# Kernel tuning notes

Measured on AMD Instinct MI355X. Metric: run time of the kernel, lower is better.

Reference implementation:

```python
import jax, jax.numpy as jnp
import numpy as np

N = 100000      # nodes
E = 1600000     # edges
IN = 64         # in_channels
ED = 16         # edge_dim
HID = 64        # hidden_dim
L = 5           # num conv layers
MLPL = 4        # linears per GINE mlp
B = 512         # num graphs
BN_EPS = 1e-5


def _linear_init(key, fan_in, shape):
    bound = 1.0 / np.sqrt(fan_in)
    return jax.random.uniform(key, shape, jnp.float32, -bound, bound)


def setup_inputs() -> dict:
    key = jax.random.key(0)
    ks = jax.random.split(key, 12)
    x = jax.random.normal(ks[0], (N, IN), jnp.float32)
    edge_index = jax.random.randint(ks[1], (2, E), 0, N)
    batch = jnp.sort(jax.random.randint(ks[2], (N,), 0, B))
    edge_attr = jax.random.normal(ks[3], (E, ED), jnp.float32)

    node_W = _linear_init(ks[4], IN, (IN, HID))
    node_b = _linear_init(ks[5], IN, (HID,))
    edge_W = _linear_init(ks[6], ED, (ED, HID))
    edge_b = _linear_init(ks[7], ED, (HID,))
    eps_arr = jnp.zeros((L,), jnp.float32)           # train_eps init = 0
    mlp_W = _linear_init(ks[8], HID, (L, MLPL, HID, HID))
    mlp_b = _linear_init(ks[9], HID, (L, MLPL, HID))
    bn_gamma = jnp.ones((L, HID), jnp.float32)
    bn_beta = jnp.zeros((L, HID), jnp.float32)

    return dict(x=x, edge_attr=edge_attr, node_W=node_W, node_b=node_b,
                edge_W=edge_W, edge_b=edge_b, eps_arr=eps_arr,
                mlp_W=mlp_W, mlp_b=mlp_b, bn_gamma=bn_gamma, bn_beta=bn_beta,
                edge_index=edge_index, batch=batch)


def _mlp(h, Ws, bs):
    # Linear,ReLU,Linear,ReLU,Linear,ReLU,Linear (make_mlp num_layers=4)
    for i in range(MLPL):
        h = h @ Ws[i] + bs[i]
        if i < MLPL - 1:
            h = jax.nn.relu(h)
    return h


def reference(x, edge_attr, node_W, node_b, edge_W, edge_b, eps_arr,
              mlp_W, mlp_b, bn_gamma, bn_beta, edge_index, batch):
    h = x @ node_W + node_b                      # [N, HID]
    e = edge_attr @ edge_W + edge_b              # [E, HID]
    src, dst = edge_index[0], edge_index[1]      # messages src -> dst
    for l in range(L):
        h_res = h
        msg = jax.nn.relu(h[src] + e)            # [E, HID] GINE message
        aggr = jax.ops.segment_sum(msg, dst, num_segments=N)
        h = _mlp((1.0 + eps_arr[l]) * h + aggr, mlp_W[l], mlp_b[l])
        mu = h.mean(axis=0)
        var = h.var(axis=0)                      # biased, matches BN training
        h = (h - mu) * jax.lax.rsqrt(var + BN_EPS) * bn_gamma[l] + bn_beta[l]
        h = jax.nn.relu(h) + h_res
    # global mean pool
    counts = jax.ops.segment_sum(jnp.ones((h.shape[0],), h.dtype), batch, num_segments=B)
    g = jax.ops.segment_sum(h, batch, num_segments=B) / jnp.clip(counts, 1.0)[:, None]
    return g
```

## Files before the change

### kernel.cpp

```cpp
#include <hip/hip_runtime.h>

typedef unsigned short u16;
typedef unsigned int u32;
typedef __attribute__((ext_vector_type(8))) short short8_t;
typedef __attribute__((ext_vector_type(4))) float f32x4;

static_assert(sizeof(short8_t) == 16, "short8 must be 16B");

#define NN 100000
#define NE 1600000

__device__ __forceinline__ float b2f(u16 s) {
    return __builtin_bit_cast(float, ((u32)s) << 16);
}
__device__ __forceinline__ u16 f2b(float f) {
    u32 u = __builtin_bit_cast(u32, f);
    u32 r = u + 0x7fffu + ((u >> 16) & 1u);
    return (u16)(r >> 16);
}
__device__ __forceinline__ u32 pack2(float a, float b) {
    return (u32)f2b(a) | ((u32)f2b(b) << 16);
}
__device__ __forceinline__ float ldf(const void* p, size_t i, int bf) {
    return bf ? b2f(((const u16*)p)[i]) : ((const float*)p)[i];
}

__global__ void detect_kernel(const u32* __restrict__ g, int* __restrict__ flag) {
    if (threadIdx.x == 0 && blockIdx.x == 0) flag[0] = (g[0] == 0x3F803F80u) ? 1 : 0;
}

__global__ __launch_bounds__(256) void hist_kernel(const int* __restrict__ dstA,
                                                   int* __restrict__ cnt, int ne) {
    int e = blockIdx.x * 256 + threadIdx.x;
    if (e >= ne) return;
    atomicAdd(&cnt[dstA[e]], 1);
}

__global__ __launch_bounds__(256) void scanA_kernel(const int* __restrict__ cnt,
                                                    int* __restrict__ tmp,
                                                    int* __restrict__ bsum, int n) {
    __shared__ int sm[2][512];
    int t = threadIdx.x;
    int b0 = blockIdx.x * 512;
    sm[0][t] = (b0 + t < n) ? cnt[b0 + t] : 0;
    sm[0][t + 256] = (b0 + t + 256 < n) ? cnt[b0 + t + 256] : 0;
    int pp = 0;
    for (int off = 1; off < 512; off <<= 1) {
        __syncthreads();
        int j0 = t, j1 = t + 256;
        sm[pp ^ 1][j0] = sm[pp][j0] + (j0 >= off ? sm[pp][j0 - off] : 0);
        sm[pp ^ 1][j1] = sm[pp][j1] + (j1 >= off ? sm[pp][j1 - off] : 0);
        pp ^= 1;
    }
    __syncthreads();
    if (b0 + t < n) tmp[b0 + t] = sm[pp][t];
    if (b0 + t + 256 < n) tmp[b0 + t + 256] = sm[pp][t + 256];
    if (t == 0) bsum[blockIdx.x] = sm[pp][511];
}

__global__ __launch_bounds__(256) void scanB_kernel(int* __restrict__ bsum, int nb) {
    __shared__ int sm[2][256];
    int t = threadIdx.x;
    sm[0][t] = (t < nb) ? bsum[t] : 0;
    int pp = 0;
    for (int off = 1; off < 256; off <<= 1) {
        __syncthreads();
        sm[pp ^ 1][t] = sm[pp][t] + (t >= off ? sm[pp][t - off] : 0);
        pp ^= 1;
    }
    __syncthreads();
    bsum[t] = (t == 0) ? 0 : sm[pp][t - 1];
}

__global__ __launch_bounds__(256) void scanC_kernel(const int* __restrict__ tmp,
                                                    const int* __restrict__ bsum,
                                                    int* __restrict__ row_start, int n, int ne) {
    int i = blockIdx.x * 256 + threadIdx.x;
    if (i > n) return;
    if (i == n) { row_start[n] = ne; return; }
    int off = bsum[i >> 9];
    int loc = i & 511;
    row_start[i] = off + (loc ? tmp[i - 1] : 0);
}

__global__ __launch_bounds__(256) void scatter_kernel(const int* __restrict__ srcA,
                                                      const int* __restrict__ dstA,
                                                      int* __restrict__ cursor,
                                                      int* __restrict__ sperm,
                                                      int* __restrict__ eidx, int ne) {
    int e = blockIdx.x * 256 + threadIdx.x;
    if (e >= ne) return;
    int d = dstA[e];
    int pos = atomicAdd(&cursor[d], 1);
    sperm[pos] = srcA[e];
    eidx[pos] = e;
}

__global__ __launch_bounds__(256) void eperm_kernel(const void* __restrict__ edge_attr,
                                                    const void* __restrict__ eW,
                                                    const void* __restrict__ eB,
                                                    const int* __restrict__ eidx,
                                                    u16* __restrict__ ec, int ne,
                                                    const int* __restrict__ flagp) {
    int bf = flagp[0];
    int lane = threadIdx.x & 63;
    int m = lane & 15;
    int quad = lane >> 4;
    int wid = (blockIdx.x * 256 + threadIdx.x) >> 6;
    int nw = gridDim.x * 4;
    short8_t bfr[4];
    float bsv[4];
#pragma unroll
    for (int t = 0; t < 4; t++) {
        short8_t f;
#pragma unroll
        for (int j = 0; j < 8; j++) {
            int k = quad * 8 + j;
            u16 wv = 0;
            if (k < 16) wv = f2b(ldf(eW, (size_t)k * 64 + t * 16 + m, bf));
            f[j] = (short)wv;
        }
        bfr[t] = f;
        bsv[t] = ldf(eB, t * 16 + m, bf);
    }
    int ngroups = (ne + 15) >> 4;
    for (int g = wid; g < ngroups; g += nw) {
        int row = g * 16 + m;
        int eid = (row < ne) ? eidx[row] : 0;
        short8_t afr = {0, 0, 0, 0, 0, 0, 0, 0};
        if (quad < 2) {
            if (bf) {
                const u16* ap = (const u16*)edge_attr + (size_t)eid * 16 + quad * 8;
                afr = *(const short8_t*)ap;
            } else {
                const float* ap = (const float*)edge_attr + (size_t)eid * 16 + quad * 8;
                float4 q0 = *(const float4*)ap;
                float4 q1 = *(const float4*)(ap + 4);
                afr[0] = (short)f2b(q0.x); afr[1] = (short)f2b(q0.y);
                afr[2] = (short)f2b(q0.z); afr[3] = (short)f2b(q0.w);
                afr[4] = (short)f2b(q1.x); afr[5] = (short)f2b(q1.y);
                afr[6] = (short)f2b(q1.z); afr[7] = (short)f2b(q1.w);
            }
        }
        f32x4 acc[4];
#pragma unroll
        for (int t = 0; t < 4; t++) {
            f32x4 a;
            a[0] = bsv[t]; a[1] = bsv[t]; a[2] = bsv[t]; a[3] = bsv[t];
            acc[t] = __builtin_amdgcn_mfma_f32_16x16x32_bf16(afr, bfr[t], a, 0, 0, 0);
        }
        int rbase = g * 16 + quad * 4;
#pragma unroll
        for (int t = 0; t < 4; t++)
#pragma unroll
            for (int r = 0; r < 4; r++) {
                int rr = rbase + r;
                if (rr < ne) ec[(size_t)rr * 64 + t * 16 + m] = f2b(acc[t][r]);
            }
    }
}

__global__ __launch_bounds__(256) void eacopy_kernel(const void* __restrict__ edge_attr,
                                                     const int* __restrict__ eidx,
                                                     u16* __restrict__ eap, int ne,
                                                     const int* __restrict__ flagp) {
    int bf = flagp[0];
    long long t = (long long)blockIdx.x * 256 + threadIdx.x;
    if (t >= (long long)ne * 16) return;
    int j = (int)(t >> 4), c = (int)(t & 15);
    int eid = eidx[j];
    eap[(size_t)j * 16 + c] = f2b(ldf(edge_attr, (size_t)eid * 16 + c, bf));
}

template <int NLIN, bool STATS, bool INEXT, bool OUTB16>
__global__ __launch_bounds__(256) void linear64_kernel(const void* in, float* out, u16* outb,
                                                       const void* __restrict__ W, size_t w_off,
                                                       const void* __restrict__ bias,
                                                       size_t b_off, float* stats, int n,
                                                       const int* __restrict__ flagp) {
    __shared__ __align__(16) u16 Ab[2][64 * 72];
    const int bf = flagp[0];
    const int tid = threadIdx.x;
    const int lane = tid & 63;
    const int w = tid >> 6;
    const int m = lane & 15;
    const int quad = lane >> 4;
    const int col = w * 16 + m;
    short8_t bfr[NLIN][2];
    float bsv[NLIN];
#pragma unroll
    for (int i = 0; i < NLIN; i++) {
        bsv[i] = ldf(bias, b_off + i * 64 + col, bf);
#pragma unroll
        for (int kk = 0; kk < 2; kk++) {
            short8_t f;
#pragma unroll
            for (int j = 0; j < 8; j++) {
                size_t idx = w_off + (size_t)i * 4096 + (size_t)(kk * 32 + quad * 8 + j) * 64 + col;
                u16 wv = bf ? ((const u16*)W)[idx] : f2b(((const float*)W)[idx]);
                f[j] = (short)wv;
            }
            bfr[i][kk] = f;
        }
    }
    const int srow = tid >> 2;
    const int sc0 = (tid & 3) << 4;
    const int ntiles = (n + 63) >> 6;
    for (int tile = blockIdx.x; tile < ntiles; tile += gridDim.x) {
        const int base = tile * 64;
        __syncthreads();
        {
            int gr = base + srow;
            uint4 w0 = make_uint4(0, 0, 0, 0), w1 = make_uint4(0, 0, 0, 0);
            if (gr < n) {
                if (INEXT && bf) {
                    const uint4* gp = (const uint4*)((const u16*)in + (size_t)gr * 64 + sc0);
                    w0 = gp[0];
                    w1 = gp[1];
                } else {
                    const float4* gp = (const float4*)((const float*)in + (size_t)gr * 64 + sc0);
                    float4 q0 = gp[0], q1 = gp[1], q2 = gp[2], q3 = gp[3];
                    w0.x = pack2(q0.x, q0.y); w0.y = pack2(q0.z, q0.w);
                    w0.z = pack2(q1.x, q1.y); w0.w = pack2(q1.z, q1.w);
                    w1.x = pack2(q2.x, q2.y); w1.y = pack2(q2.z, q2.w);
                    w1.z = pack2(q3.x, q3.y); w1.w = pack2(q3.z, q3.w);
                }
            }
            uint4* lp = (uint4*)&Ab[0][srow * 72 + sc0];
            lp[0] = w0;
            lp[1] = w1;
        }
        __syncthreads();
        int cur = 0;
#pragma unroll
        for (int i = 0; i < NLIN; i++) {
            f32x4 accT[4];
#pragma unroll
            for (int t = 0; t < 4; t++) {
                f32x4 acc;
                acc[0] = bsv[i]; acc[1] = bsv[i]; acc[2] = bsv[i]; acc[3] = bsv[i];
                int r = t * 16 + m;
                const u16* ap = &Ab[cur][r * 72 + quad * 8];
                short8_t a0 = *(const short8_t*)ap;
                short8_t a1 = *(const short8_t*)(ap + 32);
                acc = __builtin_amdgcn_mfma_f32_16x16x32_bf16(a0, bfr[i][0], acc, 0, 0, 0);
                acc = __builtin_amdgcn_mfma_f32_16x16x32_bf16(a1, bfr[i][1], acc, 0, 0, 0);
                accT[t] = acc;
            }
            if (i < NLIN - 1) {
#pragma unroll
                for (int t = 0; t < 4; t++)
#pragma unroll
                    for (int reg = 0; reg < 4; reg++) {
                        int r2 = t * 16 + quad * 4 + reg;
                        Ab[cur ^ 1][r2 * 72 + col] = f2b(fmaxf(accT[t][reg], 0.f));
                    }
                __syncthreads();
                cur ^= 1;
            } else {
                float s1 = 0.f, s2 = 0.f;
#pragma unroll
                for (int t = 0; t < 4; t++)
#pragma unroll
                    for (int reg = 0; reg < 4; reg++) {
                        int gr = base + t * 16 + quad * 4 + reg;
                        if (gr < n) {
                            float v = accT[t][reg];
                            out[(size_t)gr * 64 + col] = v;
                            if (OUTB16) outb[(size_t)gr * 64 + col] = f2b(v);
                            if (STATS) { s1 += v; s2 += v * v; }
                        }
                    }
                if (STATS) {
                    s1 += __shfl_xor(s1, 16, 64);
                    s2 += __shfl_xor(s2, 16, 64);
                    s1 += __shfl_xor(s1, 32, 64);
                    s2 += __shfl_xor(s2, 32, 64);
                    if (quad == 0) {
                        atomicAdd(&stats[col], s1);
                        atomicAdd(&stats[64 + col], s2);
                    }
                }
            }
        }
    }
}

template <bool EC>
__global__ __launch_bounds__(256) void agg_kernel(const float* __restrict__ h,
                                                  const u16* __restrict__ hb,
                                                  const u16* __restrict__ ec,
                                                  const int* __restrict__ sperm,
                                                  const int* __restrict__ row_start,
                                                  const void* __restrict__ eps_arr, int layer,
                                                  float* __restrict__ u, int n,
                                                  const void* __restrict__ eW,
                                                  const void* __restrict__ eB,
                                                  const int* __restrict__ flagp) {
    int bf = flagp[0];
    int lane = threadIdx.x & 63;
    int i = blockIdx.x * 4 + (threadIdx.x >> 6);
    if (i >= n) return;
    float wt[16];
    float ebv = 0.f;
    if (!EC) {
#pragma unroll
        for (int k = 0; k < 16; k++) wt[k] = ldf(eW, k * 64 + lane, bf);
        ebv = ldf(eB, lane, bf);
    }
    int beg = row_start[i], end = row_start[i + 1];
    float acc = 0.f;
    if (EC) {
        int p = beg;
        for (; p + 3 < end; p += 4) {
            int s0 = sperm[p], s1 = sperm[p + 1], s2 = sperm[p + 2], s3 = sperm[p + 3];
            float h0 = b2f(hb[(size_t)s0 * 64 + lane]);
            float h1 = b2f(hb[(size_t)s1 * 64 + lane]);
            float h2 = b2f(hb[(size_t)s2 * 64 + lane]);
            float h3 = b2f(hb[(size_t)s3 * 64 + lane]);
            float e0 = b2f(ec[(size_t)p * 64 + lane]);
            float e1 = b2f(ec[(size_t)(p + 1) * 64 + lane]);
            float e2 = b2f(ec[(size_t)(p + 2) * 64 + lane]);
            float e3 = b2f(ec[(size_t)(p + 3) * 64 + lane]);
            acc += fmaxf(h0 + e0, 0.f);
            acc += fmaxf(h1 + e1, 0.f);
            acc += fmaxf(h2 + e2, 0.f);
            acc += fmaxf(h3 + e3, 0.f);
        }
        for (; p < end; ++p) {
            int s0 = sperm[p];
            acc += fmaxf(b2f(hb[(size_t)s0 * 64 + lane]) + b2f(ec[(size_t)p * 64 + lane]), 0.f);
        }
    } else {
        for (int p = beg; p < end; ++p) {
            int s0 = sperm[p];
            float hv = b2f(hb[(size_t)s0 * 64 + lane]);
            float eav = 0.f;
            if (lane < 16) eav = b2f(ec[(size_t)p * 16 + lane]);
            float ev = ebv;
#pragma unroll
            for (int k = 0; k < 16; k++) {
                int bits = __builtin_amdgcn_readlane(__builtin_bit_cast(int, eav), k);
                ev += __builtin_bit_cast(float, bits) * wt[k];
            }
            acc += fmaxf(hv + ev, 0.f);
        }
    }
    float eps = 1.f + ldf(eps_arr, layer, bf);
    u[(size_t)i * 64 + lane] = eps * h[(size_t)i * 64 + lane] + acc;
}

__global__ __launch_bounds__(256) void bnres_kernel(const float* __restrict__ v,
                                                    float* __restrict__ h, u16* __restrict__ hb,
                                                    const float* __restrict__ stats,
                                                    const void* __restrict__ gamma,
                                                    const void* __restrict__ beta, size_t g_off,
                                                    int n, const int* __restrict__ flagp) {
    int bf = flagp[0];
    size_t base = ((size_t)blockIdx.x * 256 + threadIdx.x) * 4;
    if (base >= (size_t)n * 64) return;
    int f0 = (int)(base & 63);
    float inv = 1.f / (float)n;
    float4 vv = *(const float4*)(v + base);
    float4 hh = *(const float4*)(h + base);
    float vs[4] = {vv.x, vv.y, vv.z, vv.w};
    float hs[4] = {hh.x, hh.y, hh.z, hh.w};
    float res[4];
    u16 pb[4];
#pragma unroll
    for (int j = 0; j < 4; j++) {
        int f = f0 + j;
        float mu = stats[f] * inv;
        float var = stats[64 + f] * inv - mu * mu;
        float rs = rsqrtf(var + 1e-5f);
        float ga = ldf(gamma, g_off + f, bf), be = ldf(beta, g_off + f, bf);
        float y = (vs[j] - mu) * rs * ga + be;
        float hn = fmaxf(y, 0.f) + hs[j];
        res[j] = hn;
        pb[j] = f2b(hn);
    }
    float4 ro;
    ro.x = res[0]; ro.y = res[1]; ro.z = res[2]; ro.w = res[3];
    *(float4*)(h + base) = ro;
    uint2 po;
    po.x = (u32)pb[0] | ((u32)pb[1] << 16);
    po.y = (u32)pb[2] | ((u32)pb[3] << 16);
    *(uint2*)(hb + base) = po;
}

__global__ __launch_bounds__(256) void pool1_kernel(const float* __restrict__ h,
                                                    const int* __restrict__ batch,
                                                    float* __restrict__ gsum,
                                                    float* __restrict__ gcnt, int n) {
    int lane = threadIdx.x & 63;
    int s = blockIdx.x * 4 + (threadIdx.x >> 6);
    int start = s * 256;
    if (start >= n) return;
    int endn = min(start + 256, n);
    int cur = -1;
    float acc = 0.f, c = 0.f;
    for (int m = start; m < endn; ++m) {
        int b = batch[m];
        if (b != cur) {
            if (cur >= 0) {
                atomicAdd(&gsum[cur * 64 + lane], acc);
                if (lane == 0) atomicAdd(&gcnt[cur], c);
            }
            cur = b;
            acc = 0.f;
            c = 0.f;
        }
        acc += h[(size_t)m * 64 + lane];
        c += 1.f;
    }
    if (cur >= 0) {
        atomicAdd(&gsum[cur * 64 + lane], acc);
        if (lane == 0) atomicAdd(&gcnt[cur], c);
    }
}

__global__ __launch_bounds__(256) void pool2_kernel(const float* __restrict__ gsum,
                                                    const float* __restrict__ gcnt,
                                                    float* __restrict__ out) {
    int idx = blockIdx.x * 256 + threadIdx.x;
    if (idx >= 512 * 64) return;
    int b = idx >> 6;
    out[idx] = gsum[idx] / fmaxf(gcnt[b], 1.f);
}

extern "C" void kernel_launch(void* const* d_in, const int* in_sizes, int n_in, void* d_out,
                              int out_size, void* d_ws, size_t ws_size, hipStream_t stream) {
    const int N = NN, E = NE;
    const void* x = d_in[0];
    const void* edge_attr = d_in[1];
    const void* node_W = d_in[2];
    const void* node_b = d_in[3];
    const void* edge_W = d_in[4];
    const void* edge_b = d_in[5];
    const void* eps_arr = d_in[6];
    const void* mlp_W = d_in[7];
    const void* mlp_b = d_in[8];
    const void* bn_gamma = d_in[9];
    const void* bn_beta = d_in[10];
    const int* edge_index = (const int*)d_in[11];
    const int* batch = (const int*)d_in[12];

    char* ws = (char*)d_ws;
    size_t o = 0;
    auto take = [&](size_t bytes) -> size_t {
        size_t r = o;
        o = (o + bytes + 255) & ~(size_t)255;
        return r;
    };
    size_t cnt_o = take((size_t)N * 4);
    size_t stats_o = take(5 * 128 * 4);
    size_t gsum_o = take(512 * 64 * 4);
    size_t gcnt_o = take(512 * 4);
    size_t zero_len = o;
    size_t flag_o = take(256);
    size_t row_o = take((size_t)(N + 1) * 4);
    size_t tmp_o = take((size_t)N * 4);
    size_t bsum_o = take(256 * 4);
    size_t cur_o = take((size_t)N * 4);
    size_t sperm_o = take((size_t)E * 4);
    size_t eidx_o = take((size_t)E * 4);
    size_t h_o = take((size_t)N * 64 * 4);
    size_t hb_o = take((size_t)N * 64 * 2);
    size_t u_o = take((size_t)N * 64 * 4);
    size_t ec_o = o;
    bool EC = ws_size >= ec_o + (size_t)E * 64 * 2;

    int* cnt = (int*)(ws + cnt_o);
    float* stats = (float*)(ws + stats_o);
    float* gsum = (float*)(ws + gsum_o);
    float* gcnt = (float*)(ws + gcnt_o);
    int* flagp = (int*)(ws + flag_o);
    int* row = (int*)(ws + row_o);
    int* tmp = (int*)(ws + tmp_o);
    int* bsum = (int*)(ws + bsum_o);
    int* curs = (int*)(ws + cur_o);
    int* sperm = (int*)(ws + sperm_o);
    int* eidx = (int*)(ws + eidx_o);
    float* h = (float*)(ws + h_o);
    u16* hb = (u16*)(ws + hb_o);
    float* u = (float*)(ws + u_o);
    u16* ecache = (u16*)(ws + ec_o);

    hipMemsetAsync(ws, 0, zero_len, stream);
    detect_kernel<<<1, 64, 0, stream>>>((const u32*)bn_gamma, flagp);
    const int* srcA = edge_index;
    const int* dstA = edge_index + E;

    hist_kernel<<<E / 256, 256, 0, stream>>>(dstA, cnt, E);
    int nb = (N + 511) / 512;
    scanA_kernel<<<nb, 256, 0, stream>>>(cnt, tmp, bsum, N);
    scanB_kernel<<<1, 256, 0, stream>>>(bsum, nb);
    scanC_kernel<<<(N + 256) / 256, 256, 0, stream>>>(tmp, bsum, row, N, E);
    hipMemcpyAsync(curs, row, (size_t)N * 4, hipMemcpyDeviceToDevice, stream);
    scatter_kernel<<<E / 256, 256, 0, stream>>>(srcA, dstA, curs, sperm, eidx, E);

    if (EC)
        eperm_kernel<<<2048, 256, 0, stream>>>(edge_attr, edge_W, edge_b, eidx, ecache, E, flagp);
    else
        eacopy_kernel<<<(E * 16) / 256, 256, 0, stream>>>(edge_attr, eidx, ecache, E, flagp);

    linear64_kernel<1, false, true, true><<<784, 256, 0, stream>>>(
        x, h, hb, node_W, 0, node_b, 0, nullptr, N, flagp);

    for (int l = 0; l < 5; l++) {
        if (EC)
            agg_kernel<true><<<N / 4, 256, 0, stream>>>(h, hb, ecache, sperm, row, eps_arr, l, u,
                                                        N, edge_W, edge_b, flagp);
        else
            agg_kernel<false><<<N / 4, 256, 0, stream>>>(h, hb, ecache, sperm, row, eps_arr, l, u,
                                                         N, edge_W, edge_b, flagp);
        linear64_kernel<4, true, false, false><<<784, 256, 0, stream>>>(
            u, u, nullptr, mlp_W, (size_t)l * 4 * 4096, mlp_b, (size_t)l * 256,
            stats + l * 128, N, flagp);
        bnres_kernel<<<(N * 64 / 4 + 255) / 256, 256, 0, stream>>>(
            u, h, hb, stats + l * 128, bn_gamma, bn_beta, (size_t)l * 64, N, flagp);
    }

    pool1_kernel<<<(N + 1023) / 1024, 256, 0, stream>>>(h, batch, gsum, gcnt, N);
    pool2_kernel<<<(512 * 64) / 256, 256, 0, stream>>>(gsum, gcnt, (float*)d_out);
}
```

Measured before the change: 1.629 ms.

## Switch aggregation to edge-balanced chunks with atomic boundary merges

The per-node aggregation kernel becomes an edge-parallel kernel. Each wave handles a fixed chunk of dst-sorted edges, accumulates runs with the same destination, and merges chunk-boundary partial sums with atomics. The (1+eps)*h self term is now written ahead of time into u by the producing kernel (node linear or BN-residual), which lets aggregation accumulate in place. Smaller changes fold the cursor copy into the scan kernel and process two edge groups per iteration in the edge-projection kernel. The aim is load balance independent of node degree; the cost is an extra dperm array, atomic traffic, and extra writes of u.

```diff
diff --git a/kernel.cpp b/kernel.cpp
--- a/kernel.cpp
+++ b/kernel.cpp
@@ -9,6 +9,7 @@
 
 #define NN 100000
 #define NE 1600000
+#define CH 128
 
 __device__ __forceinline__ float b2f(u16 s) {
     return __builtin_bit_cast(float, ((u32)s) << 16);
@@ -74,26 +75,64 @@
 
 __global__ __launch_bounds__(256) void scanC_kernel(const int* __restrict__ tmp,
                                                     const int* __restrict__ bsum,
-                                                    int* __restrict__ row_start, int n, int ne) {
+                                                    int* __restrict__ row_start,
+                                                    int* __restrict__ curs, int n, int ne) {
     int i = blockIdx.x * 256 + threadIdx.x;
     if (i > n) return;
     if (i == n) { row_start[n] = ne; return; }
     int off = bsum[i >> 9];
     int loc = i & 511;
-    row_start[i] = off + (loc ? tmp[i - 1] : 0);
+    int v = off + (loc ? tmp[i - 1] : 0);
+    row_start[i] = v;
+    curs[i] = v;
 }
 
 __global__ __launch_bounds__(256) void scatter_kernel(const int* __restrict__ srcA,
                                                       const int* __restrict__ dstA,
                                                       int* __restrict__ cursor,
                                                       int* __restrict__ sperm,
+                                                      int* __restrict__ dperm,
                                                       int* __restrict__ eidx, int ne) {
     int e = blockIdx.x * 256 + threadIdx.x;
     if (e >= ne) return;
     int d = dstA[e];
     int pos = atomicAdd(&cursor[d], 1);
     sperm[pos] = srcA[e];
+    dperm[pos] = d;
     eidx[pos] = e;
+}
+
+__device__ __forceinline__ short8_t load_afr(const void* __restrict__ edge_attr,
+                                             const int* __restrict__ eidx, int row, int ne,
+                                             int quad, int bf) {
+    short8_t afr = {0, 0, 0, 0, 0, 0, 0, 0};
+    int eid = (row < ne) ? eidx[row] : 0;
+    if (quad < 2) {
+        if (bf) {
+            afr = *(const short8_t*)((const u16*)edge_attr + (size_t)eid * 16 + quad * 8);
+        } else {
+            const float* ap = (const float*)edge_attr + (size_t)eid * 16 + quad * 8;
+            float4 q0 = *(const float4*)ap;
+            float4 q1 = *(const float4*)(ap + 4);
+            afr[0] = (short)f2b(q0.x); afr[1] = (short)f2b(q0.y);
+            afr[2] = (short)f2b(q0.z); afr[3] = (short)f2b(q0.w);
+            afr[4] = (short)f2b(q1.x); afr[5] = (short)f2b(q1.y);
+            afr[6] = (short)f2b(q1.z); afr[7] = (short)f2b(q1.w);
+        }
+    }
+    return afr;
+}
+
+__device__ __forceinline__ void store_ec(u16* __restrict__ ec, const f32x4* acc, int g, int quad,
+                                         int m, int ne) {
+    int rbase = g * 16 + quad * 4;
+#pragma unroll
+    for (int t = 0; t < 4; t++)
+#pragma unroll
+        for (int r = 0; r < 4; r++) {
+            int rr = rbase + r;
+            if (rr < ne) ec[(size_t)rr * 64 + t * 16 + m] = f2b(acc[t][r]);
+        }
 }
 
 __global__ __launch_bounds__(256) void eperm_kernel(const void* __restrict__ edge_attr,
@@ -124,39 +163,23 @@
         bsv[t] = ldf(eB, t * 16 + m, bf);
     }
     int ngroups = (ne + 15) >> 4;
-    for (int g = wid; g < ngroups; g += nw) {
-        int row = g * 16 + m;
-        int eid = (row < ne) ? eidx[row] : 0;
-        short8_t afr = {0, 0, 0, 0, 0, 0, 0, 0};
-        if (quad < 2) {
-            if (bf) {
-                const u16* ap = (const u16*)edge_attr + (size_t)eid * 16 + quad * 8;
-                afr = *(const short8_t*)ap;
-            } else {
-                const float* ap = (const float*)edge_attr + (size_t)eid * 16 + quad * 8;
-                float4 q0 = *(const float4*)ap;
-                float4 q1 = *(const float4*)(ap + 4);
-                afr[0] = (short)f2b(q0.x); afr[1] = (short)f2b(q0.y);
-                afr[2] = (short)f2b(q0.z); afr[3] = (short)f2b(q0.w);
-                afr[4] = (short)f2b(q1.x); afr[5] = (short)f2b(q1.y);
-                afr[6] = (short)f2b(q1.z); afr[7] = (short)f2b(q1.w);
-            }
-        }
-        f32x4 acc[4];
+    int npairs = (ngroups + 1) >> 1;
+    for (int gp = wid; gp < npairs; gp += nw) {
+        int ga = gp * 2, gb = gp * 2 + 1;
+        short8_t afrA = load_afr(edge_attr, eidx, ga * 16 + m, ne, quad, bf);
+        short8_t afrB = {0, 0, 0, 0, 0, 0, 0, 0};
+        bool hasB = (gb < ngroups);
+        if (hasB) afrB = load_afr(edge_attr, eidx, gb * 16 + m, ne, quad, bf);
+        f32x4 accA[4], accB[4];
 #pragma unroll
         for (int t = 0; t < 4; t++) {
             f32x4 a;
             a[0] = bsv[t]; a[1] = bsv[t]; a[2] = bsv[t]; a[3] = bsv[t];
-            acc[t] = __builtin_amdgcn_mfma_f32_16x16x32_bf16(afr, bfr[t], a, 0, 0, 0);
-        }
-        int rbase = g * 16 + quad * 4;
-#pragma unroll
-        for (int t = 0; t < 4; t++)
-#pragma unroll
-            for (int r = 0; r < 4; r++) {
-                int rr = rbase + r;
-                if (rr < ne) ec[(size_t)rr * 64 + t * 16 + m] = f2b(acc[t][r]);
-            }
+            accA[t] = __builtin_amdgcn_mfma_f32_16x16x32_bf16(afrA, bfr[t], a, 0, 0, 0);
+            accB[t] = __builtin_amdgcn_mfma_f32_16x16x32_bf16(afrB, bfr[t], a, 0, 0, 0);
+        }
+        store_ec(ec, accA, ga, quad, m, ne);
+        if (hasB) store_ec(ec, accB, gb, quad, m, ne);
     }
 }
 
@@ -172,12 +195,15 @@
     eap[(size_t)j * 16 + c] = f2b(ldf(edge_attr, (size_t)eid * 16 + c, bf));
 }
 
-template <int NLIN, bool STATS, bool INEXT, bool OUTB16>
+template <int NLIN, bool STATS, bool INEXT, bool OUTB16, bool UINIT>
 __global__ __launch_bounds__(256) void linear64_kernel(const void* in, float* out, u16* outb,
                                                        const void* __restrict__ W, size_t w_off,
                                                        const void* __restrict__ bias,
                                                        size_t b_off, float* stats, int n,
-                                                       const int* __restrict__ flagp) {
+                                                       const int* __restrict__ flagp,
+                                                       float* uinit,
+                                                       const void* __restrict__ eps_arr,
+                                                       int eps_idx) {
     __shared__ __align__(16) u16 Ab[2][64 * 72];
     const int bf = flagp[0];
     const int tid = threadIdx.x;
@@ -186,6 +212,8 @@
     const int m = lane & 15;
     const int quad = lane >> 4;
     const int col = w * 16 + m;
+    float epsv = 0.f;
+    if (UINIT) epsv = 1.f + ldf(eps_arr, eps_idx, bf);
     short8_t bfr[NLIN][2];
     float bsv[NLIN];
 #pragma unroll
@@ -268,6 +296,7 @@
                             float v = accT[t][reg];
                             out[(size_t)gr * 64 + col] = v;
                             if (OUTB16) outb[(size_t)gr * 64 + col] = f2b(v);
+                            if (UINIT) uinit[(size_t)gr * 64 + col] = epsv * v;
                             if (STATS) { s1 += v; s2 += v * v; }
                         }
                     }
@@ -286,86 +315,114 @@
     }
 }
 
-template <bool EC>
-__global__ __launch_bounds__(256) void agg_kernel(const float* __restrict__ h,
-                                                  const u16* __restrict__ hb,
-                                                  const u16* __restrict__ ec,
-                                                  const int* __restrict__ sperm,
-                                                  const int* __restrict__ row_start,
-                                                  const void* __restrict__ eps_arr, int layer,
-                                                  float* __restrict__ u, int n,
-                                                  const void* __restrict__ eW,
-                                                  const void* __restrict__ eB,
-                                                  const int* __restrict__ flagp) {
+__global__ __launch_bounds__(256) void agg2_kernel(const u16* __restrict__ hb,
+                                                   const u16* __restrict__ ec,
+                                                   const int* __restrict__ sperm,
+                                                   const int* __restrict__ dperm,
+                                                   float* u, int ne) {
+    int lane = threadIdx.x & 63;
+    int wv = blockIdx.x * 4 + (threadIdx.x >> 6);
+    int p0 = wv * CH;
+    if (p0 >= ne) return;
+    int pend = min(p0 + CH, ne);
+    int cur = dperm[p0];
+    float acc = 0.f;
+    bool first = true;
+    int p = p0;
+    for (; p + 3 < pend; p += 4) {
+        int4 s4 = *(const int4*)(sperm + p);
+        int4 d4 = *(const int4*)(dperm + p);
+        float hv[4], ev[4];
+        hv[0] = b2f(hb[(size_t)s4.x * 64 + lane]);
+        hv[1] = b2f(hb[(size_t)s4.y * 64 + lane]);
+        hv[2] = b2f(hb[(size_t)s4.z * 64 + lane]);
+        hv[3] = b2f(hb[(size_t)s4.w * 64 + lane]);
+        ev[0] = b2f(ec[(size_t)p * 64 + lane]);
+        ev[1] = b2f(ec[(size_t)(p + 1) * 64 + lane]);
+        ev[2] = b2f(ec[(size_t)(p + 2) * 64 + lane]);
+        ev[3] = b2f(ec[(size_t)(p + 3) * 64 + lane]);
+        int ds[4] = {d4.x, d4.y, d4.z, d4.w};
+#pragma unroll
+        for (int j = 0; j < 4; j++) {
+            if (ds[j] != cur) {
+                float* up = &u[(size_t)cur * 64 + lane];
+                if (first) atomicAdd(up, acc);
+                else *up += acc;
+                first = false;
+                cur = ds[j];
+                acc = 0.f;
+            }
+            acc += fmaxf(hv[j] + ev[j], 0.f);
+        }
+    }
+    for (; p < pend; ++p) {
+        int s = sperm[p], d = dperm[p];
+        if (d != cur) {
+            float* up = &u[(size_t)cur * 64 + lane];
+            if (first) atomicAdd(up, acc);
+            else *up += acc;
+            first = false;
+            cur = d;
+            acc = 0.f;
+        }
+        acc += fmaxf(b2f(hb[(size_t)s * 64 + lane]) + b2f(ec[(size_t)p * 64 + lane]), 0.f);
+    }
+    atomicAdd(&u[(size_t)cur * 64 + lane], acc);
+}
+
+__global__ __launch_bounds__(256) void aggF_kernel(const u16* __restrict__ hb,
+                                                   const u16* __restrict__ ec,
+                                                   const int* __restrict__ sperm,
+                                                   const int* __restrict__ row_start,
+                                                   float* u, int n,
+                                                   const void* __restrict__ eW,
+                                                   const void* __restrict__ eB,
+                                                   const int* __restrict__ flagp) {
     int bf = flagp[0];
     int lane = threadIdx.x & 63;
     int i = blockIdx.x * 4 + (threadIdx.x >> 6);
     if (i >= n) return;
     float wt[16];
-    float ebv = 0.f;
-    if (!EC) {
-#pragma unroll
-        for (int k = 0; k < 16; k++) wt[k] = ldf(eW, k * 64 + lane, bf);
-        ebv = ldf(eB, lane, bf);
-    }
+#pragma unroll
+    for (int k = 0; k < 16; k++) wt[k] = ldf(eW, k * 64 + lane, bf);
+    float ebv = ldf(eB, lane, bf);
     int beg = row_start[i], end = row_start[i + 1];
     float acc = 0.f;
-    if (EC) {
-        int p = beg;
-        for (; p + 3 < end; p += 4) {
-            int s0 = sperm[p], s1 = sperm[p + 1], s2 = sperm[p + 2], s3 = sperm[p + 3];
-            float h0 = b2f(hb[(size_t)s0 * 64 + lane]);
-            float h1 = b2f(hb[(size_t)s1 * 64 + lane]);
-            float h2 = b2f(hb[(size_t)s2 * 64 + lane]);
-            float h3 = b2f(hb[(size_t)s3 * 64 + lane]);
-            float e0 = b2f(ec[(size_t)p * 64 + lane]);
-            float e1 = b2f(ec[(size_t)(p + 1) * 64 + lane]);
-            float e2 = b2f(ec[(size_t)(p + 2) * 64 + lane]);
-            float e3 = b2f(ec[(size_t)(p + 3) * 64 + lane]);
-            acc += fmaxf(h0 + e0, 0.f);
-            acc += fmaxf(h1 + e1, 0.f);
-            acc += fmaxf(h2 + e2, 0.f);
-            acc += fmaxf(h3 + e3, 0.f);
-        }
-        for (; p < end; ++p) {
-            int s0 = sperm[p];
-            acc += fmaxf(b2f(hb[(size_t)s0 * 64 + lane]) + b2f(ec[(size_t)p * 64 + lane]), 0.f);
-        }
-    } else {
-        for (int p = beg; p < end; ++p) {
-            int s0 = sperm[p];
-            float hv = b2f(hb[(size_t)s0 * 64 + lane]);
-            float eav = 0.f;
-            if (lane < 16) eav = b2f(ec[(size_t)p * 16 + lane]);
-            float ev = ebv;
-#pragma unroll
-            for (int k = 0; k < 16; k++) {
-                int bits = __builtin_amdgcn_readlane(__builtin_bit_cast(int, eav), k);
-                ev += __builtin_bit_cast(float, bits) * wt[k];
-            }
-            acc += fmaxf(hv + ev, 0.f);
-        }
-    }
-    float eps = 1.f + ldf(eps_arr, layer, bf);
-    u[(size_t)i * 64 + lane] = eps * h[(size_t)i * 64 + lane] + acc;
-}
-
-__global__ __launch_bounds__(256) void bnres_kernel(const float* __restrict__ v,
-                                                    float* __restrict__ h, u16* __restrict__ hb,
+    for (int p = beg; p < end; ++p) {
+        int s0 = sperm[p];
+        float hv = b2f(hb[(size_t)s0 * 64 + lane]);
+        float eav = 0.f;
+        if (lane < 16) eav = b2f(ec[(size_t)p * 16 + lane]);
+        float ev = ebv;
+#pragma unroll
+        for (int k = 0; k < 16; k++) {
+            int bits = __builtin_amdgcn_readlane(__builtin_bit_cast(int, eav), k);
+            ev += __builtin_bit_cast(float, bits) * wt[k];
+        }
+        acc += fmaxf(hv + ev, 0.f);
+    }
+    u[(size_t)i * 64 + lane] += acc;
+}
+
+__global__ __launch_bounds__(256) void bnres_kernel(float* uv, float* __restrict__ h,
+                                                    u16* __restrict__ hb,
                                                     const float* __restrict__ stats,
                                                     const void* __restrict__ gamma,
                                                     const void* __restrict__ beta, size_t g_off,
-                                                    int n, const int* __restrict__ flagp) {
+                                                    int n, const int* __restrict__ flagp,
+                                                    const void* __restrict__ eps_arr,
+                                                    int eps_next, int write_u) {
     int bf = flagp[0];
     size_t base = ((size_t)blockIdx.x * 256 + threadIdx.x) * 4;
     if (base >= (size_t)n * 64) return;
     int f0 = (int)(base & 63);
     float inv = 1.f / (float)n;
-    float4 vv = *(const float4*)(v + base);
+    float epsv = write_u ? (1.f + ldf(eps_arr, eps_next, bf)) : 0.f;
+    float4 vv = *(const float4*)(uv + base);
     float4 hh = *(const float4*)(h + base);
     float vs[4] = {vv.x, vv.y, vv.z, vv.w};
     float hs[4] = {hh.x, hh.y, hh.z, hh.w};
-    float res[4];
+    float res[4], ui[4];
     u16 pb[4];
 #pragma unroll
     for (int j = 0; j < 4; j++) {
@@ -377,6 +434,7 @@
         float y = (vs[j] - mu) * rs * ga + be;
         float hn = fmaxf(y, 0.f) + hs[j];
         res[j] = hn;
+        ui[j] = epsv * hn;
         pb[j] = f2b(hn);
     }
     float4 ro;
@@ -386,6 +444,11 @@
     po.x = (u32)pb[0] | ((u32)pb[1] << 16);
     po.y = (u32)pb[2] | ((u32)pb[3] << 16);
     *(uint2*)(hb + base) = po;
+    if (write_u) {
+        float4 uo;
+        uo.x = ui[0]; uo.y = ui[1]; uo.z = ui[2]; uo.w = ui[3];
+        *(float4*)(uv + base) = uo;
+    }
 }
 
 __global__ __launch_bounds__(256) void pool1_kernel(const float* __restrict__ h,
@@ -463,6 +526,7 @@
     size_t bsum_o = take(256 * 4);
     size_t cur_o = take((size_t)N * 4);
     size_t sperm_o = take((size_t)E * 4);
+    size_t dperm_o = take((size_t)E * 4);
     size_t eidx_o = take((size_t)E * 4);
     size_t h_o = take((size_t)N * 64 * 4);
     size_t hb_o = take((size_t)N * 64 * 2);
@@ -480,6 +544,7 @@
     int* bsum = (int*)(ws + bsum_o);
     int* curs = (int*)(ws + cur_o);
     int* sperm = (int*)(ws + sperm_o);
+    int* dperm = (int*)(ws + dperm_o);
     int* eidx = (int*)(ws + eidx_o);
     float* h = (float*)(ws + h_o);
     u16* hb = (u16*)(ws + hb_o);
@@ -495,30 +560,30 @@
     int nb = (N + 511) / 512;
     scanA_kernel<<<nb, 256, 0, stream>>>(cnt, tmp, bsum, N);
     scanB_kernel<<<1, 256, 0, stream>>>(bsum, nb);
-    scanC_kernel<<<(N + 256) / 256, 256, 0, stream>>>(tmp, bsum, row, N, E);
-    hipMemcpyAsync(curs, row, (size_t)N * 4, hipMemcpyDeviceToDevice, stream);
-    scatter_kernel<<<E / 256, 256, 0, stream>>>(srcA, dstA, curs, sperm, eidx, E);
+    scanC_kernel<<<(N + 256) / 256, 256, 0, stream>>>(tmp, bsum, row, curs, N, E);
+    scatter_kernel<<<E / 256, 256, 0, stream>>>(srcA, dstA, curs, sperm, dperm, eidx, E);
 
     if (EC)
         eperm_kernel<<<2048, 256, 0, stream>>>(edge_attr, edge_W, edge_b, eidx, ecache, E, flagp);
     else
         eacopy_kernel<<<(E * 16) / 256, 256, 0, stream>>>(edge_attr, eidx, ecache, E, flagp);
 
-    linear64_kernel<1, false, true, true><<<784, 256, 0, stream>>>(
-        x, h, hb, node_W, 0, node_b, 0, nullptr, N, flagp);
-
+    linear64_kernel<1, false, true, true, true><<<784, 256, 0, stream>>>(
+        x, h, hb, node_W, 0, node_b, 0, nullptr, N, flagp, u, eps_arr, 0);
+
+    int nchunks = (E + CH - 1) / CH;
     for (int l = 0; l < 5; l++) {
         if (EC)
-            agg_kernel<true><<<N / 4, 256, 0, stream>>>(h, hb, ecache, sperm, row, eps_arr, l, u,
-                                                        N, edge_W, edge_b, flagp);
+            agg2_kernel<<<(nchunks + 3) / 4, 256, 0, stream>>>(hb, ecache, sperm, dperm, u, E);
         else
-            agg_kernel<false><<<N / 4, 256, 0, stream>>>(h, hb, ecache, sperm, row, eps_arr, l, u,
-                                                         N, edge_W, edge_b, flagp);
-        linear64_kernel<4, true, false, false><<<784, 256, 0, stream>>>(
-            u, u, nullptr, mlp_W, (size_t)l * 4 * 4096, mlp_b, (size_t)l * 256,
-            stats + l * 128, N, flagp);
+            aggF_kernel<<<(N + 3) / 4, 256, 0, stream>>>(hb, ecache, sperm, row, u, N, edge_W,
+                                                         edge_b, flagp);
+        linear64_kernel<4, true, false, false, false><<<784, 256, 0, stream>>>(
+            u, u, nullptr, mlp_W, (size_t)l * 4 * 4096, mlp_b, (size_t)l * 256, stats + l * 128,
+            N, flagp, nullptr, eps_arr, 0);
         bnres_kernel<<<(N * 64 / 4 + 255) / 256, 256, 0, stream>>>(
-            u, h, hb, stats + l * 128, bn_gamma, bn_beta, (size_t)l * 64, N, flagp);
+            u, h, hb, stats + l * 128, bn_gamma, bn_beta, (size_t)l * 64, N, flagp, eps_arr,
+            l + 1, (l < 4) ? 1 : 0);
     }
 
     pool1_kernel<<<(N + 1023) / 1024, 256, 0, stream>>>(h, batch, gsum, gcnt, N);
```

Measured after the change: 1.655 ms. Within noise of the previous version (+1.6%).
